# Performance work log

Measured on AMD Instinct MI355X. Metric: run time of the kernel, lower is better.

The kernel has to match this reference:

```python
import jax, jax.numpy as jnp
import numpy as np

ENC_DIM = 256
DEC_DIM = 256
INT_DIM = 256


def setup_inputs() -> dict:
    key = jax.random.key(0)
    k1, k2, k3, k4, k5 = jax.random.split(key, 5)
    B, T = 64, 2048
    encoder_states = jax.random.normal(k1, (B, T, ENC_DIM), dtype=jnp.float32)
    decoder_state = jax.random.normal(k2, (B, DEC_DIM), dtype=jnp.float32)
    s1 = 1.0 / np.sqrt(ENC_DIM)
    s2 = 1.0 / np.sqrt(DEC_DIM)
    s3 = 1.0 / np.sqrt(INT_DIM)
    w1 = jax.random.uniform(k3, (INT_DIM, ENC_DIM), jnp.float32, -s1, s1)
    w2 = jax.random.uniform(k4, (INT_DIM, DEC_DIM), jnp.float32, -s2, s2)
    v = jax.random.uniform(k5, (1, INT_DIM), jnp.float32, -s3, s3)
    return {"encoder_states": encoder_states, "decoder_state": decoder_state,
            "w1": w1, "w2": w2, "v": v}


def reference(encoder_states, decoder_state, w1, w2, v):
    # scores: v @ tanh(W1 e_t + W2 d) for all t at once
    enc_proj = jnp.einsum('bte,ie->bti', encoder_states, w1)      # [B,T,I]
    dec_proj = jnp.einsum('bd,id->bi', decoder_state, w2)          # [B,I]
    scores = jnp.einsum('bti,oi->bt', jnp.tanh(enc_proj + dec_proj[:, None, :]), v)  # [B,T]
    attention_probs = jax.nn.softmax(scores, axis=1)[:, :, None]   # [B,T,1]
    final_context_vec = jnp.sum(attention_probs * encoder_states, axis=1)  # [B,E]
    return final_context_vec, attention_probs
```

## Files before the change

### kernel.cpp

```cpp
#include <hip/hip_runtime.h>
#include <hip/hip_bf16.h>
#include <math.h>

#define Bq 64
#define Tq 2048
#define Eq 256
#define Dq 256
#define Iq 256

using short8  = __attribute__((ext_vector_type(8))) short;
using floatx4 = __attribute__((ext_vector_type(4))) float;

__device__ __forceinline__ float fast_tanh(float x) {
    float e = __expf(2.0f * x);
    return 1.0f - 2.0f / (e + 1.0f);
}

__device__ __forceinline__ ushort f2bf(float x) {
    union { __hip_bfloat16 h; ushort u; } c;
    c.h = __float2bfloat16(x);
    return c.u;
}

__device__ __forceinline__ void async_load16(const void* g, void* l) {
    __builtin_amdgcn_global_load_lds(
        (const __attribute__((address_space(1))) void*)g,
        (__attribute__((address_space(3))) void*)l, 16, 0, 0);
}

__global__ __launch_bounds__(256) void prep_kernel(
    const float* __restrict__ w1, ushort* __restrict__ w1sw,
    const float* __restrict__ dec, const float* __restrict__ w2,
    float* __restrict__ dproj)
{
    if (blockIdx.x < 32) {
        const int kc = blockIdx.x;
        const int i  = threadIdx.x;
        const float* src = w1 + i * Eq + kc * 8;
        float4 f0 = *(const float4*)src;
        float4 f1 = *(const float4*)(src + 4);
        ushort u[8] = { f2bf(f0.x), f2bf(f0.y), f2bf(f0.z), f2bf(f0.w),
                        f2bf(f1.x), f2bf(f1.y), f2bf(f1.z), f2bf(f1.w) };
        *(short8*)&w1sw[(kc * 256 + i) * 8] = *(short8*)u;
    } else {
        const int b = blockIdx.x - 32;
        const int i = threadIdx.x;
        __shared__ float dls[Dq];
        dls[i] = dec[b * Dq + i];
        __syncthreads();
        const float* w2r = w2 + i * Dq;
        float acc = 0.f;
        #pragma unroll 8
        for (int d = 0; d < Dq; ++d) acc += dls[d] * w2r[d];
        dproj[b * Iq + i] = acc;
    }
}

__global__ __launch_bounds__(256) void scores_mfma_kernel(
    const float*  __restrict__ enc,
    const ushort* __restrict__ w1sw,
    const float*  __restrict__ v,
    const float*  __restrict__ dproj,
    float* __restrict__ escore,
    float* __restrict__ denom)
{
    const int b   = blockIdx.y;
    const int t0  = blockIdx.x * 64;
    const int tid = threadIdx.x;
    const int w   = tid >> 6;
    const int l   = tid & 63;
    const int l15 = l & 15;
    const int lq  = l >> 4;

    __shared__ ushort As[64 * 72];
    __shared__ ushort Bs[16384];
    __shared__ float  vls[Iq], dls[Iq];

    vls[tid] = v[tid];
    dls[tid] = dproj[b * Iq + tid];

    floatx4 acc[4][4];
    #pragma unroll
    for (int mi = 0; mi < 4; ++mi)
        #pragma unroll
        for (int ni = 0; ni < 4; ++ni)
            acc[mi][ni] = (floatx4)0.f;

    const float* encB = enc + ((size_t)b * Tq + t0) * Eq;

    for (int k0 = 0; k0 < Eq; k0 += 64) {
        const ushort* gb = w1sw + (size_t)(k0 >> 3) * 256 * 8;
        #pragma unroll
        for (int r = 0; r < 8; ++r) {
            const int qbase = r * 256 + w * 64;
            async_load16(gb + (qbase + l) * 8, Bs + qbase * 8);
        }
        #pragma unroll
        for (int r = 0; r < 4; ++r) {
            const int idx = tid + 256 * r;
            const int row = idx >> 4;
            const int c4  = (idx & 15) * 4;
            float4 f = *(const float4*)&encB[row * Eq + k0 + c4];
            ushort4 u;
            u.x = f2bf(f.x); u.y = f2bf(f.y); u.z = f2bf(f.z); u.w = f2bf(f.w);
            *(ushort4*)&As[row * 72 + c4] = u;
        }
        __syncthreads();
        #pragma unroll
        for (int ks = 0; ks < 2; ++ks) {
            const int kloc = ks * 32 + lq * 8;
            short8 af[4], bfv[4];
            #pragma unroll
            for (int mi = 0; mi < 4; ++mi)
                af[mi] = *(const short8*)&As[(mi * 16 + l15) * 72 + kloc];
            #pragma unroll
            for (int ni = 0; ni < 4; ++ni)
                bfv[ni] = *(const short8*)&Bs[((ks * 4 + lq) * 256 + w * 64 + ni * 16 + l15) * 8];
            #pragma unroll
            for (int mi = 0; mi < 4; ++mi)
                #pragma unroll
                for (int ni = 0; ni < 4; ++ni)
                    acc[mi][ni] = __builtin_amdgcn_mfma_f32_16x16x32_bf16(
                        af[mi], bfv[ni], acc[mi][ni], 0, 0, 0);
        }
        __syncthreads();
    }

    float part[4][4];
    #pragma unroll
    for (int mi = 0; mi < 4; ++mi)
        #pragma unroll
        for (int r = 0; r < 4; ++r) part[mi][r] = 0.f;

    #pragma unroll
    for (int ni = 0; ni < 4; ++ni) {
        const int i   = w * 64 + ni * 16 + l15;
        const float vi = vls[i];
        const float dp = dls[i];
        #pragma unroll
        for (int mi = 0; mi < 4; ++mi)
            #pragma unroll
            for (int r = 0; r < 4; ++r)
                part[mi][r] += vi * fast_tanh(acc[mi][ni][r] + dp);
    }

    float* red2 = (float*)Bs;
    #pragma unroll
    for (int mi = 0; mi < 4; ++mi)
        #pragma unroll
        for (int r = 0; r < 4; ++r)
            red2[(w * 64 + mi * 16 + lq * 4 + r) * 20 + l15] = part[mi][r];
    __syncthreads();

    if (tid < 64) {
        float s = 0.f;
        #pragma unroll
        for (int ww = 0; ww < 4; ++ww) {
            const float* rp = red2 + (ww * 64 + tid) * 20;
            float4 q0 = *(const float4*)(rp + 0);
            float4 q1 = *(const float4*)(rp + 4);
            float4 q2 = *(const float4*)(rp + 8);
            float4 q3 = *(const float4*)(rp + 12);
            s += (q0.x + q0.y + q0.z + q0.w) + (q1.x + q1.y + q1.z + q1.w)
               + (q2.x + q2.y + q2.z + q2.w) + (q3.x + q3.y + q3.z + q3.w);
        }
        const float es = __expf(s);
        escore[(size_t)b * Tq + t0 + tid] = es;
        float tot = es;
        tot += __shfl_xor(tot, 1);  tot += __shfl_xor(tot, 2);
        tot += __shfl_xor(tot, 4);  tot += __shfl_xor(tot, 8);
        tot += __shfl_xor(tot, 16); tot += __shfl_xor(tot, 32);
        if (tid == 0) atomicAdd(&denom[b], tot);
    }
}

__global__ __launch_bounds__(256) void context_kernel(
    const float* __restrict__ enc, const float* __restrict__ escore,
    const float* __restrict__ denom,
    float* __restrict__ probs, float* __restrict__ ctx)
{
    const int b   = blockIdx.y;
    const int t0  = blockIdx.x * 256;
    const int tid = threadIdx.x;
    const int tg  = tid >> 6;
    const int e4  = (tid & 63) * 4;

    __shared__ float pv[256];
    __shared__ float red[4][256];

    const float inv = 1.0f / denom[b];
    const float p = escore[(size_t)b * Tq + t0 + tid] * inv;
    pv[tid] = p;
    probs[(size_t)b * Tq + t0 + tid] = p;
    __syncthreads();

    const float* encB = enc + ((size_t)b * Tq + t0) * Eq;
    float4 a = {0.f, 0.f, 0.f, 0.f};
    #pragma unroll 4
    for (int tt = 0; tt < 64; ++tt) {
        const int t = tt * 4 + tg;
        const float pt = pv[t];
        float4 ev = *(const float4*)&encB[t * Eq + e4];
        a.x += pt * ev.x; a.y += pt * ev.y; a.z += pt * ev.z; a.w += pt * ev.w;
    }
    *(float4*)&red[tg][e4] = a;
    __syncthreads();
    if (tg == 0) {
        float4 a0 = *(const float4*)&red[0][e4];
        float4 a1 = *(const float4*)&red[1][e4];
        float4 a2 = *(const float4*)&red[2][e4];
        float4 a3 = *(const float4*)&red[3][e4];
        float* c = ctx + b * Eq + e4;
        atomicAdd(c + 0, a0.x + a1.x + a2.x + a3.x);
        atomicAdd(c + 1, a0.y + a1.y + a2.y + a3.y);
        atomicAdd(c + 2, a0.z + a1.z + a2.z + a3.z);
        atomicAdd(c + 3, a0.w + a1.w + a2.w + a3.w);
    }
}

extern "C" void kernel_launch(void* const* d_in, const int* in_sizes, int n_in,
                              void* d_out, int out_size, void* d_ws, size_t ws_size,
                              hipStream_t stream) {
    const float* enc = (const float*)d_in[0];
    const float* dec = (const float*)d_in[1];
    const float* w1  = (const float*)d_in[2];
    const float* w2  = (const float*)d_in[3];
    const float* v   = (const float*)d_in[4];

    float* out   = (float*)d_out;
    float* ctx   = out;
    float* probs = out + Bq * Eq;

    char* ws = (char*)d_ws;
    float*  dproj = (float*)ws;
    ushort* w1sw  = (ushort*)(ws + 262144);
    float*  denom = (float*)(ws + 262144 + 131072);

    hipMemsetAsync(ctx, 0, Bq * Eq * sizeof(float), stream);
    hipMemsetAsync(denom, 0, Bq * sizeof(float), stream);

    prep_kernel<<<dim3(96), dim3(256), 0, stream>>>(w1, w1sw, dec, w2, dproj);
    scores_mfma_kernel<<<dim3(Tq / 64, Bq), dim3(256), 0, stream>>>(
        enc, w1sw, v, dproj, probs, denom);
    context_kernel<<<dim3(Tq / 256, Bq), dim3(256), 0, stream>>>(
        enc, probs, denom, probs, ctx);
}
```

Baseline: 254.2 us.

## Fuse context accumulation into scores kernel with per-tile partials and finalize pass

New measurement: 233.5 us. -8.1%, faster.

```diff
diff --git a/kernel.cpp b/kernel.cpp
--- a/kernel.cpp
+++ b/kernel.cpp
@@ -56,16 +56,18 @@
     }
 }
 
-__global__ __launch_bounds__(256) void scores_mfma_kernel(
+__global__ __launch_bounds__(256) void scores_ctx_kernel(
     const float*  __restrict__ enc,
     const ushort* __restrict__ w1sw,
     const float*  __restrict__ v,
     const float*  __restrict__ dproj,
     float* __restrict__ escore,
-    float* __restrict__ denom)
+    float* __restrict__ ctxp,
+    float* __restrict__ denomp)
 {
     const int b   = blockIdx.y;
-    const int t0  = blockIdx.x * 64;
+    const int bx  = blockIdx.x;
+    const int t0  = bx * 64;
     const int tid = threadIdx.x;
     const int w   = tid >> 6;
     const int l   = tid & 63;
@@ -75,6 +77,7 @@
     __shared__ ushort As[64 * 72];
     __shared__ ushort Bs[16384];
     __shared__ float  vls[Iq], dls[Iq];
+    __shared__ float  pv[64];
 
     vls[tid] = v[tid];
     dls[tid] = dproj[b * Iq + tid];
@@ -165,57 +168,68 @@
                + (q2.x + q2.y + q2.z + q2.w) + (q3.x + q3.y + q3.z + q3.w);
         }
         const float es = __expf(s);
+        pv[tid] = es;
         escore[(size_t)b * Tq + t0 + tid] = es;
         float tot = es;
         tot += __shfl_xor(tot, 1);  tot += __shfl_xor(tot, 2);
         tot += __shfl_xor(tot, 4);  tot += __shfl_xor(tot, 8);
         tot += __shfl_xor(tot, 16); tot += __shfl_xor(tot, 32);
-        if (tid == 0) atomicAdd(&denom[b], tot);
-    }
-}
-
-__global__ __launch_bounds__(256) void context_kernel(
-    const float* __restrict__ enc, const float* __restrict__ escore,
-    const float* __restrict__ denom,
+        if (tid == 0) denomp[bx * Bq + b] = tot;
+    }
+    __syncthreads();
+
+    const int tg = tid >> 6;
+    const int el = (tid & 63) * 4;
+    float4 a = {0.f, 0.f, 0.f, 0.f};
+    #pragma unroll 4
+    for (int tt = 0; tt < 16; ++tt) {
+        const int t = tg * 16 + tt;
+        const float pt = pv[t];
+        float4 ev = *(const float4*)&encB[t * Eq + el];
+        a.x += pt * ev.x; a.y += pt * ev.y; a.z += pt * ev.z; a.w += pt * ev.w;
+    }
+    float* redf = (float*)As;
+    *(float4*)&redf[tg * 256 + el] = a;
+    __syncthreads();
+    if (tg == 0) {
+        float4 a0 = *(const float4*)&redf[0 * 256 + el];
+        float4 a1 = *(const float4*)&redf[1 * 256 + el];
+        float4 a2 = *(const float4*)&redf[2 * 256 + el];
+        float4 a3 = *(const float4*)&redf[3 * 256 + el];
+        float4 o;
+        o.x = a0.x + a1.x + a2.x + a3.x;
+        o.y = a0.y + a1.y + a2.y + a3.y;
+        o.z = a0.z + a1.z + a2.z + a3.z;
+        o.w = a0.w + a1.w + a2.w + a3.w;
+        *(float4*)&ctxp[((size_t)bx * Bq + b) * Eq + el] = o;
+    }
+}
+
+__global__ __launch_bounds__(256) void finalize_kernel(
+    const float* __restrict__ ctxp, const float* __restrict__ denomp,
     float* __restrict__ probs, float* __restrict__ ctx)
 {
-    const int b   = blockIdx.y;
-    const int t0  = blockIdx.x * 256;
+    const int b   = blockIdx.x;
     const int tid = threadIdx.x;
-    const int tg  = tid >> 6;
-    const int e4  = (tid & 63) * 4;
-
-    __shared__ float pv[256];
-    __shared__ float red[4][256];
-
-    const float inv = 1.0f / denom[b];
-    const float p = escore[(size_t)b * Tq + t0 + tid] * inv;
-    pv[tid] = p;
-    probs[(size_t)b * Tq + t0 + tid] = p;
-    __syncthreads();
-
-    const float* encB = enc + ((size_t)b * Tq + t0) * Eq;
-    float4 a = {0.f, 0.f, 0.f, 0.f};
-    #pragma unroll 4
-    for (int tt = 0; tt < 64; ++tt) {
-        const int t = tt * 4 + tg;
-        const float pt = pv[t];
-        float4 ev = *(const float4*)&encB[t * Eq + e4];
-        a.x += pt * ev.x; a.y += pt * ev.y; a.z += pt * ev.z; a.w += pt * ev.w;
-    }
-    *(float4*)&red[tg][e4] = a;
-    __syncthreads();
-    if (tg == 0) {
-        float4 a0 = *(const float4*)&red[0][e4];
-        float4 a1 = *(const float4*)&red[1][e4];
-        float4 a2 = *(const float4*)&red[2][e4];
-        float4 a3 = *(const float4*)&red[3][e4];
-        float* c = ctx + b * Eq + e4;
-        atomicAdd(c + 0, a0.x + a1.x + a2.x + a3.x);
-        atomicAdd(c + 1, a0.y + a1.y + a2.y + a3.y);
-        atomicAdd(c + 2, a0.z + a1.z + a2.z + a3.z);
-        atomicAdd(c + 3, a0.w + a1.w + a2.w + a3.w);
-    }
+
+    float d = denomp[(tid & 31) * Bq + b];
+    d += __shfl_xor(d, 1);  d += __shfl_xor(d, 2);  d += __shfl_xor(d, 4);
+    d += __shfl_xor(d, 8);  d += __shfl_xor(d, 16);
+    const float inv = 1.0f / d;
+
+    float* prow = probs + (size_t)b * Tq + tid * 8;
+    float4 p0 = *(const float4*)(prow + 0);
+    float4 p1 = *(const float4*)(prow + 4);
+    p0.x *= inv; p0.y *= inv; p0.z *= inv; p0.w *= inv;
+    p1.x *= inv; p1.y *= inv; p1.z *= inv; p1.w *= inv;
+    *(float4*)(prow + 0) = p0;
+    *(float4*)(prow + 4) = p1;
+
+    float s = 0.f;
+    #pragma unroll 8
+    for (int c = 0; c < 32; ++c)
+        s += ctxp[((size_t)c * Bq + b) * Eq + tid];
+    ctx[b * Eq + tid] = s * inv;
 }
 
 extern "C" void kernel_launch(void* const* d_in, const int* in_sizes, int n_in,
@@ -232,16 +246,13 @@
     float* probs = out + Bq * Eq;
 
     char* ws = (char*)d_ws;
-    float*  dproj = (float*)ws;
-    ushort* w1sw  = (ushort*)(ws + 262144);
-    float*  denom = (float*)(ws + 262144 + 131072);
-
-    hipMemsetAsync(ctx, 0, Bq * Eq * sizeof(float), stream);
-    hipMemsetAsync(denom, 0, Bq * sizeof(float), stream);
+    float*  ctxp   = (float*)ws;
+    float*  denomp = (float*)(ws + (32*Bq*Eq)*4);
+    float*  dproj  = (float*)(ws + (32*Bq*Eq)*4 + 32*Bq*4);
+    ushort* w1sw   = (ushort*)(ws + (32*Bq*Eq)*4 + 32*Bq*4 + Bq*Iq*4);
 
     prep_kernel<<<dim3(96), dim3(256), 0, stream>>>(w1, w1sw, dec, w2, dproj);
-    scores_mfma_kernel<<<dim3(Tq / 64, Bq), dim3(256), 0, stream>>>(
-        enc, w1sw, v, dproj, probs, denom);
-    context_kernel<<<dim3(Tq / 256, Bq), dim3(256), 0, stream>>>(
-        enc, probs, denom, probs, ctx);
-}
+    scores_ctx_kernel<<<dim3(Tq / 64, Bq), dim3(256), 0, stream>>>(
+        enc, w1sw, v, dproj, probs, ctxp, denomp);
+    finalize_kernel<<<dim3(Bq), dim3(256), 0, stream>>>(ctxp, denomp, probs, ctx);
+}
```
